# Performance work log

Hardware: AMD Instinct MI355X
Metric: run time of the kernel (lower is better)

Reference implementation:

```python
import jax, jax.numpy as jnp
import numpy as np

N, D, P = 131072, 128, 512
COMMIT_W = 0.1
ENT_LAMBDA = 200000.0


def setup_inputs() -> dict:
    key = jax.random.key(0)
    k1, k2 = jax.random.split(key)
    input_data = jax.random.normal(k1, (N, D), dtype=jnp.float32)
    # codebook init matches torch: uniform(-1/p, 1/p)
    codebook = jax.random.uniform(k2, (P, D), dtype=jnp.float32, minval=-1.0 / P, maxval=1.0 / P)
    return {"input_data": input_data, "codebook": codebook}


def _inv_cov(codebook):
    # full covariance of codebook rows (torch.no_grad -> stop_gradient)
    p, d = codebook.shape
    mu = codebook.mean(axis=0, keepdims=True)
    c = codebook - mu
    cov = (c.T @ c) / (p - 1) + 1e-3 * jnp.eye(d, dtype=codebook.dtype)
    return jax.lax.stop_gradient(jnp.linalg.inv(cov))


def reference(input_data, codebook):
    p, d = codebook.shape
    inv_cov = _inv_cov(codebook)

    # Mahalanobis distances via quadratic-form expansion (no [N,p,d] intermediate):
    xS = input_data @ inv_cov                      # [N, d]
    xq = jnp.sum(xS * input_data, axis=1)          # [N]
    cS = codebook @ inv_cov                        # [p, d]
    cq = jnp.sum(cS * codebook, axis=1)            # [p]
    distances = xq[:, None] - 2.0 * (xS @ codebook.T) + cq[None, :]  # [N, p]

    idx = jnp.argmin(distances, axis=1)            # [N]
    quantized = jnp.take(codebook, idx, axis=0)    # [N, d] (== one_hot @ codebook)

    def batch_mahal(x, y):
        diff = x - y
        return jnp.mean(jnp.sum((diff @ inv_cov) * diff, axis=1))

    codebook_loss = batch_mahal(jax.lax.stop_gradient(quantized), input_data)
    commitment_loss = COMMIT_W * batch_mahal(quantized, jax.lax.stop_gradient(input_data))

    # codebook usage entropy regularizer
    counts = jnp.zeros((p,), dtype=input_data.dtype).at[idx].add(1.0)
    probs = counts / (counts.sum() + 1e-8)
    entropy = -jnp.sum(probs * jnp.log(probs + 1e-8))
    codebook_loss = codebook_loss - ENT_LAMBDA * entropy

    # straight-through estimator
    quantized_st = input_data + jax.lax.stop_gradient(quantized - input_data)
    return quantized_st, commitment_loss, codebook_loss, idx
```

## Files before the change

kernel.cpp:

```cpp
#include <hip/hip_runtime.h>


typedef _Float16 half8 __attribute__((ext_vector_type(8)));
typedef float floatx4 __attribute__((ext_vector_type(4)));

#define NROWS 131072
#define DIM 128
#define NCODE 512
#define ND 16777216

#define WS_LH    0
#define WS_CH    32768
#define WS_W     163840
#define WS_SH    294912
#define WS_CQ    327680
#define WS_CNT   329728
#define WS_SUMS  346112

#define MFMA16(A, B, C) __builtin_amdgcn_mfma_f32_16x16x32_f16(A, B, C, 0, 0, 0)

__device__ __forceinline__ int moff(int row, int colh) {
  return row * 256 + ((((row & 7) << 4) ^ (colh * 2)));
}

__device__ __forceinline__ void stage4k(const char* src, char* ldsbase,
                                        int w, int lane) {
  __builtin_amdgcn_global_load_lds(
      (const __attribute__((address_space(1))) void*)(src + (w * 1024 + lane * 16)),
      (__attribute__((address_space(3))) void*)(ldsbase + w * 1024),
      16, 0, 0);
}

__global__ __launch_bounds__(256) void k_prep1(
    const float* __restrict__ cb, _Float16* __restrict__ Lh,
    unsigned* __restrict__ cnt, float* __restrict__ sums) {
  __shared__ float mu[128];
  __shared__ float red[256];
  __shared__ float colI[2][512];
  __shared__ float csh[2];

  const int t = threadIdx.x, b = blockIdx.x;
  const int j = t & 127, h = t >> 7;

  if (b < 8) {
    cnt[b * 512 + t] = 0u;
    cnt[b * 512 + 256 + t] = 0u;
  }
  if (b == 8) sums[t] = 0.f;

  float sm = 0.f, sf = 0.f;
  for (int p = 0; p < 256; ++p) {
    float v = cb[(h * 256 + p) * DIM + j];
    sm += v;
    sf += v * v;
  }
  red[t] = sm;
  for (int k = t; k < 1024; k += 256)
    colI[k >> 9][k & 511] = cb[(k & 511) * DIM + 2 * b + (k >> 9)];
  __syncthreads();
  if (t < 128) mu[t] = (red[t] + red[t + 128]) * (1.f / 512.f);
  __syncthreads();
  red[t] = sf - ((t < 128) ? 512.f * mu[t] * mu[t] : 0.f);
  __syncthreads();
  for (int k = 128; k > 0; k >>= 1) {
    if (t < k) red[t] += red[t + k];
    __syncthreads();
  }
  if (t == 0) {
    float tr = red[0] * (1.f / 511.f) + 0.128f;
    csh[0] = 128.f / tr;
    csh[1] = sqrtf(128.f / tr);
  }
  __syncthreads();
  const float c = csh[0], rc = csh[1];

  const int i = 2 * b + h;
  float g = 0.f;
  for (int q = 0; q < 512; ++q) g += colI[h][q] * cb[q * DIM + j];
  float lv = rc * (((i == j) ? (1.5f - 5e-4f * c) : 0.f) -
                   (c / 1022.f) * (g - 512.f * mu[i] * mu[j]));
  *(_Float16*)((char*)Lh + moff(i, j)) = (_Float16)lv;
}

__global__ __launch_bounds__(256) void k_prep2(
    const float* __restrict__ cb, const _Float16* __restrict__ Lh,
    _Float16* __restrict__ Ch, float* __restrict__ cqb) {
  __shared__ float cqpart[16][4];
  const int t = threadIdx.x;
  const int w = t >> 6, lane = t & 63, quad = lane >> 4, l16 = lane & 15;
  const int p0 = blockIdx.x * 16;

  half8 a[4];
#pragma unroll
  for (int ci = 0; ci < 4; ++ci) {
    const float4* v = (const float4*)(cb + (p0 + l16) * DIM + ci * 32 + quad * 8);
    float4 v0 = v[0], v1 = v[1];
    half8 hh;
    hh[0] = (_Float16)v0.x; hh[1] = (_Float16)v0.y;
    hh[2] = (_Float16)v0.z; hh[3] = (_Float16)v0.w;
    hh[4] = (_Float16)v1.x; hh[5] = (_Float16)v1.y;
    hh[6] = (_Float16)v1.z; hh[7] = (_Float16)v1.w;
    a[ci] = hh;
  }
  float sq[4] = {0.f, 0.f, 0.f, 0.f};
#pragma unroll
  for (int t2 = 0; t2 < 2; ++t2) {
    const int tile = w * 2 + t2;
    floatx4 s = {0.f, 0.f, 0.f, 0.f};
#pragma unroll
    for (int ci = 0; ci < 4; ++ci) {
      half8 bb = *(const half8*)((const char*)Lh +
                                 moff(tile * 16 + l16, ci * 32 + quad * 8));
      s = MFMA16(a[ci], bb, s);
    }
#pragma unroll
    for (int r = 0; r < 4; ++r) {
      *(_Float16*)((char*)Ch + moff(p0 + quad * 4 + r, tile * 16 + l16)) =
          (_Float16)s[r];
      sq[r] += s[r] * s[r];
    }
  }
#pragma unroll
  for (int r = 0; r < 4; ++r) {
    float v = sq[r];
    v += __shfl_xor(v, 1); v += __shfl_xor(v, 2);
    v += __shfl_xor(v, 4); v += __shfl_xor(v, 8);
    sq[r] = v;
  }
  if (l16 == 0)
#pragma unroll
    for (int r = 0; r < 4; ++r) cqpart[quad * 4 + r][w] = sq[r];
  __syncthreads();
  if (t < 16)
    cqb[p0 + t] = 1024.f - 0.5f * (cqpart[t][0] + cqpart[t][1] +
                                   cqpart[t][2] + cqpart[t][3]);
}

__global__ __launch_bounds__(256) void k_prep3(
    const _Float16* __restrict__ Lh, const _Float16* __restrict__ Ch,
    _Float16* __restrict__ W, _Float16* __restrict__ Sh) {
  const int t = threadIdx.x;
  const int w = t >> 6, lane = t & 63, quad = lane >> 4, l16 = lane & 15;
  const bool isW = blockIdx.x < 32;
  const int p0 = (isW ? blockIdx.x : (blockIdx.x - 32)) * 16;
  const char* Asrc = isW ? (const char*)Ch : (const char*)Lh;
  char* Dst = isW ? (char*)W : (char*)Sh;

  half8 a[4];
#pragma unroll
  for (int ci = 0; ci < 4; ++ci)
    a[ci] = *(const half8*)(Asrc + moff(p0 + l16, ci * 32 + quad * 8));
#pragma unroll
  for (int t2 = 0; t2 < 2; ++t2) {
    const int tile = w * 2 + t2;
    floatx4 s = {0.f, 0.f, 0.f, 0.f};
#pragma unroll
    for (int ci = 0; ci < 4; ++ci) {
      half8 bb = *(const half8*)((const char*)Lh +
                                 moff(tile * 16 + l16, ci * 32 + quad * 8));
      s = MFMA16(a[ci], bb, s);
    }
#pragma unroll
    for (int r = 0; r < 4; ++r)
      *(_Float16*)(Dst + moff(p0 + quad * 4 + r, tile * 16 + l16)) =
          (_Float16)s[r];
  }
}

__global__ __launch_bounds__(256, 3) void k_main(
    const float* __restrict__ X, const float* __restrict__ cb,
    const _Float16* __restrict__ Sh, const _Float16* __restrict__ W,
    const float* __restrict__ cqb, float* __restrict__ out,
    unsigned* __restrict__ cnt, float* __restrict__ sums) {
  __shared__ __align__(16) char Xs[32768];
  __shared__ __align__(16) char Bst[2][4096];

  const int tid = threadIdx.x;
  const int w = tid >> 6, lane = tid & 63;
  const int quad = lane >> 4, l16 = lane & 15;
  const int R0 = blockIdx.x * 128;
  const int rep = blockIdx.x & 7;
  const int r0 = w * 32;
  const int brot = (blockIdx.x >> 3) & 31;

  const char* ShB = (const char*)Sh;
  const char* WB = (const char*)W;

  {
    const float4* src = (const float4*)(X + (size_t)R0 * DIM);
#pragma unroll
    for (int it = 0; it < 8; ++it) {
      int g = it * 256 + tid;
      int row = g >> 4, c8 = g & 15;
      float4 v0 = src[g * 2];
      float4 v1 = src[g * 2 + 1];
      half8 hh;
      hh[0] = (_Float16)v0.x; hh[1] = (_Float16)v0.y;
      hh[2] = (_Float16)v0.z; hh[3] = (_Float16)v0.w;
      hh[4] = (_Float16)v1.x; hh[5] = (_Float16)v1.y;
      hh[6] = (_Float16)v1.z; hh[7] = (_Float16)v1.w;
      *(half8*)(Xs + moff(row, c8 * 8)) = hh;
    }
  }

  stage4k(ShB, Bst[0], w, lane);
  __syncthreads();

  half8 a0[4], a1[4];
#pragma unroll
  for (int ci = 0; ci < 4; ++ci) {
    a0[ci] = *(const half8*)(Xs + moff(r0 + l16, ci * 32 + quad * 8));
    a1[ci] = *(const half8*)(Xs + moff(r0 + 16 + l16, ci * 32 + quad * 8));
  }

  float y2 = 0.f;
  float m0[4] = {0.f, 0.f, 0.f, 0.f}, m1[4] = {0.f, 0.f, 0.f, 0.f};

  for (int v = 0; v < 40; ++v) {
    if (v < 39) {
      const char* nsrc = (v + 1 < 8)
                             ? (ShB + (size_t)(v + 1) * 4096)
                             : (WB + (size_t)((v + 1 - 8 + brot) & 31) * 4096);
      stage4k(nsrc, Bst[(v + 1) & 1], w, lane);
    }

    const char* lb = Bst[v & 1];
    half8 bb[4];
#pragma unroll
    for (int ci = 0; ci < 4; ++ci)
      bb[ci] = *(const half8*)(lb + moff(l16, ci * 32 + quad * 8));

    if (v < 8) {
      floatx4 s0a = {0.f, 0.f, 0.f, 0.f}, s0b = {0.f, 0.f, 0.f, 0.f};
      floatx4 s1a = {0.f, 0.f, 0.f, 0.f}, s1b = {0.f, 0.f, 0.f, 0.f};
      __builtin_amdgcn_s_setprio(1);
      s0a = MFMA16(a0[0], bb[0], s0a); s0b = MFMA16(a0[1], bb[1], s0b);
      s1a = MFMA16(a1[0], bb[0], s1a); s1b = MFMA16(a1[1], bb[1], s1b);
      s0a = MFMA16(a0[2], bb[2], s0a); s0b = MFMA16(a0[3], bb[3], s0b);
      s1a = MFMA16(a1[2], bb[2], s1a); s1b = MFMA16(a1[3], bb[3], s1b);
      __builtin_amdgcn_s_setprio(0);
      const int col = v * 16 + l16;
#pragma unroll
      for (int r = 0; r < 4; ++r) {
        float xv0 = (float)*(const _Float16*)(Xs + moff(r0 + quad * 4 + r, col));
        float xv1 = (float)*(const _Float16*)(Xs + moff(r0 + 16 + quad * 4 + r, col));
        y2 += (s0a[r] + s0b[r]) * xv0 + (s1a[r] + s1b[r]) * xv1;
      }
    } else {
      const int tt = (v - 8 + brot) & 31;
      const float iv = cqb[tt * 16 + l16];
      floatx4 s0a = {iv, iv, iv, iv}, s0b = {0.f, 0.f, 0.f, 0.f};
      floatx4 s1a = {iv, iv, iv, iv}, s1b = {0.f, 0.f, 0.f, 0.f};
      __builtin_amdgcn_s_setprio(1);
      s0a = MFMA16(a0[0], bb[0], s0a); s0b = MFMA16(a0[1], bb[1], s0b);
      s1a = MFMA16(a1[0], bb[0], s1a); s1b = MFMA16(a1[1], bb[1], s1b);
      s0a = MFMA16(a0[2], bb[2], s0a); s0b = MFMA16(a0[3], bb[3], s0b);
      s1a = MFMA16(a1[2], bb[2], s1a); s1b = MFMA16(a1[3], bb[3], s1b);
      __builtin_amdgcn_s_setprio(0);
      const unsigned tag = 511u - (unsigned)(tt * 16 + l16);
#pragma unroll
      for (int r = 0; r < 4; ++r) {
        float v0 = s0a[r] + s0b[r], v1 = s1a[r] + s1b[r];
        unsigned u0 = ((__float_as_uint(v0) + 0x100u) & 0xFFFFFE00u) | tag;
        unsigned u1 = ((__float_as_uint(v1) + 0x100u) & 0xFFFFFE00u) | tag;
        m0[r] = fmaxf(m0[r], __uint_as_float(u0));
        m1[r] = fmaxf(m1[r], __uint_as_float(u1));
      }
    }
    __syncthreads();
  }

#pragma unroll
  for (int r = 0; r < 4; ++r) {
#pragma unroll
    for (int msk = 1; msk < 16; msk <<= 1) {
      m0[r] = fmaxf(m0[r], __shfl_xor(m0[r], msk));
      m1[r] = fmaxf(m1[r], __shfl_xor(m1[r], msk));
    }
  }

  float contrib = y2;
  if (l16 == 0) {
#pragma unroll
    for (int r = 0; r < 4; ++r) {
      contrib -= 2.f * (__uint_as_float(__float_as_uint(m0[r]) & 0xFFFFFE00u) - 1024.f);
      contrib -= 2.f * (__uint_as_float(__float_as_uint(m1[r]) & 0xFFFFFE00u) - 1024.f);
    }
  }
#pragma unroll
  for (int msk = 1; msk < 64; msk <<= 1) contrib += __shfl_xor(contrib, msk);
  if (lane == 0) unsafeAtomicAdd(&sums[rep * 32], contrib);

  {
    const float4* cb4 = (const float4*)cb;
    float4* out4 = (float4*)out;
#pragma unroll
    for (int r = 0; r < 4; ++r) {
      const int j0 = 511 - (int)(__float_as_uint(m0[r]) & 511u);
      const int j1 = 511 - (int)(__float_as_uint(m1[r]) & 511u);
      const int row0 = R0 + r0 + quad * 4 + r, row1 = row0 + 16;
      out4[(size_t)row0 * 32 + l16 * 2]     = cb4[(size_t)j0 * 32 + l16 * 2];
      out4[(size_t)row0 * 32 + l16 * 2 + 1] = cb4[(size_t)j0 * 32 + l16 * 2 + 1];
      out4[(size_t)row1 * 32 + l16 * 2]     = cb4[(size_t)j1 * 32 + l16 * 2];
      out4[(size_t)row1 * 32 + l16 * 2 + 1] = cb4[(size_t)j1 * 32 + l16 * 2 + 1];
      if (l16 == 0) {
        out[ND + 2 + row0] = (float)j0;
        out[ND + 2 + row1] = (float)j1;
        atomicAdd(&cnt[rep * 512 + j0], 1u);
        atomicAdd(&cnt[rep * 512 + j1], 1u);
      }
    }
  }
}

__global__ void k_final(const unsigned* __restrict__ cnt,
                        const float* __restrict__ sums, float* __restrict__ out) {
  __shared__ double sd[256];
  int t = threadIdx.x;
  double e = 0.0;
  for (int c = t; c < NCODE; c += 256) {
    unsigned u = 0;
#pragma unroll
    for (int r = 0; r < 8; ++r) u += cnt[r * 512 + c];
    float p = (float)u * (1.0f / 131072.0f);
    e += (double)(p * logf(p + 1e-8f));
  }
  sd[t] = e;
  __syncthreads();
  for (int k = 128; k > 0; k >>= 1) {
    if (t < k) sd[t] += sd[t + k];
    __syncthreads();
  }
  if (t == 0) {
    double ent = -sd[0];
    float st = 0.f;
#pragma unroll
    for (int r = 0; r < 8; ++r) st += sums[r * 32];
    double M = (double)st / 131072.0;
    out[ND] = (float)(0.1 * M);
    out[ND + 1] = (float)(M - 200000.0 * ent);
  }
}

extern "C" void kernel_launch(void* const* d_in, const int* in_sizes, int n_in,
                              void* d_out, int out_size, void* d_ws, size_t ws_size,
                              hipStream_t stream) {
  const float* X = (const float*)d_in[0];
  const float* cb = (const float*)d_in[1];
  char* ws = (char*)d_ws;
  _Float16* Lh = (_Float16*)(ws + WS_LH);
  _Float16* Ch = (_Float16*)(ws + WS_CH);
  _Float16* W = (_Float16*)(ws + WS_W);
  _Float16* Sh = (_Float16*)(ws + WS_SH);
  float* cqb = (float*)(ws + WS_CQ);
  unsigned* cnt = (unsigned*)(ws + WS_CNT);
  float* sums = (float*)(ws + WS_SUMS);
  float* out = (float*)d_out;

  k_prep1<<<64, 256, 0, stream>>>(cb, Lh, cnt, sums);
  k_prep2<<<32, 256, 0, stream>>>(cb, Lh, Ch, cqb);
  k_prep3<<<40, 256, 0, stream>>>(Lh, Ch, W, Sh);
  k_main<<<1024, 256, 0, stream>>>(X, cb, Sh, W, cqb, out, cnt, sums);
  k_final<<<1, 256, 0, stream>>>(cnt, sums, out);
}
```

Measured before the change: 166.8 us.

## Stage full W codebook in LDS once per 1024-thread block and fuse prep kernels

The main kernel now uses 1024-thread blocks that load the whole 128 KB fp16 W matrix into LDS once, instead of double-buffering 4 KB tiles with a barrier every iteration. X rows go straight from global memory into registers, and the Sh quadratic term reads Sh and X directly from global memory. The second and third prep kernels are merged into one launch, which removes a launch and a dependency step. In exchange, 128 KB of LDS per block limits occupancy to one block per CU and gives 256 blocks in total. The merge also looks racy: W is computed from Ch in the same kernel that writes Ch, relying on the block's own rows, and it reads Lh rows that other blocks wrote in the previous kernel.

```diff
diff --git a/kernel.cpp b/kernel.cpp
--- a/kernel.cpp
+++ b/kernel.cpp
@@ -23,14 +23,6 @@
   return row * 256 + ((((row & 7) << 4) ^ (colh * 2)));
 }
 
-__device__ __forceinline__ void stage4k(const char* src, char* ldsbase,
-                                        int w, int lane) {
-  __builtin_amdgcn_global_load_lds(
-      (const __attribute__((address_space(1))) void*)(src + (w * 1024 + lane * 16)),
-      (__attribute__((address_space(3))) void*)(ldsbase + w * 1024),
-      16, 0, 0);
-}
-
 __global__ __launch_bounds__(256) void k_prep1(
     const float* __restrict__ cb, _Float16* __restrict__ Lh,
     unsigned* __restrict__ cnt, float* __restrict__ sums) {
@@ -82,12 +74,38 @@
   *(_Float16*)((char*)Lh + moff(i, j)) = (_Float16)lv;
 }
 
-__global__ __launch_bounds__(256) void k_prep2(
+__global__ __launch_bounds__(256) void k_prep23(
     const float* __restrict__ cb, const _Float16* __restrict__ Lh,
-    _Float16* __restrict__ Ch, float* __restrict__ cqb) {
+    _Float16* __restrict__ Ch, _Float16* __restrict__ W,
+    _Float16* __restrict__ Sh, float* __restrict__ cqb) {
   __shared__ float cqpart[16][4];
   const int t = threadIdx.x;
   const int w = t >> 6, lane = t & 63, quad = lane >> 4, l16 = lane & 15;
+
+  if (blockIdx.x >= 32) {
+    const int p0 = (blockIdx.x - 32) * 16;
+    half8 a[4];
+#pragma unroll
+    for (int ci = 0; ci < 4; ++ci)
+      a[ci] = *(const half8*)((const char*)Lh + moff(p0 + l16, ci * 32 + quad * 8));
+#pragma unroll
+    for (int t2 = 0; t2 < 2; ++t2) {
+      const int tile = w * 2 + t2;
+      floatx4 s = {0.f, 0.f, 0.f, 0.f};
+#pragma unroll
+      for (int ci = 0; ci < 4; ++ci) {
+        half8 bb = *(const half8*)((const char*)Lh +
+                                   moff(tile * 16 + l16, ci * 32 + quad * 8));
+        s = MFMA16(a[ci], bb, s);
+      }
+#pragma unroll
+      for (int r = 0; r < 4; ++r)
+        *(_Float16*)((char*)Sh + moff(p0 + quad * 4 + r, tile * 16 + l16)) =
+            (_Float16)s[r];
+    }
+    return;
+  }
+
   const int p0 = blockIdx.x * 16;
 
   half8 a[4];
@@ -134,22 +152,11 @@
   if (t < 16)
     cqb[p0 + t] = 1024.f - 0.5f * (cqpart[t][0] + cqpart[t][1] +
                                    cqpart[t][2] + cqpart[t][3]);
-}
-
-__global__ __launch_bounds__(256) void k_prep3(
-    const _Float16* __restrict__ Lh, const _Float16* __restrict__ Ch,
-    _Float16* __restrict__ W, _Float16* __restrict__ Sh) {
-  const int t = threadIdx.x;
-  const int w = t >> 6, lane = t & 63, quad = lane >> 4, l16 = lane & 15;
-  const bool isW = blockIdx.x < 32;
-  const int p0 = (isW ? blockIdx.x : (blockIdx.x - 32)) * 16;
-  const char* Asrc = isW ? (const char*)Ch : (const char*)Lh;
-  char* Dst = isW ? (char*)W : (char*)Sh;
-
-  half8 a[4];
+
+  half8 a2[4];
 #pragma unroll
   for (int ci = 0; ci < 4; ++ci)
-    a[ci] = *(const half8*)(Asrc + moff(p0 + l16, ci * 32 + quad * 8));
+    a2[ci] = *(const half8*)((const char*)Ch + moff(p0 + l16, ci * 32 + quad * 8));
 #pragma unroll
   for (int t2 = 0; t2 < 2; ++t2) {
     const int tile = w * 2 + t2;
@@ -158,116 +165,106 @@
     for (int ci = 0; ci < 4; ++ci) {
       half8 bb = *(const half8*)((const char*)Lh +
                                  moff(tile * 16 + l16, ci * 32 + quad * 8));
-      s = MFMA16(a[ci], bb, s);
+      s = MFMA16(a2[ci], bb, s);
     }
 #pragma unroll
     for (int r = 0; r < 4; ++r)
-      *(_Float16*)(Dst + moff(p0 + quad * 4 + r, tile * 16 + l16)) =
+      *(_Float16*)((char*)W + moff(p0 + quad * 4 + r, tile * 16 + l16)) =
           (_Float16)s[r];
   }
 }
 
-__global__ __launch_bounds__(256, 3) void k_main(
+__global__ __launch_bounds__(1024, 4) void k_main(
     const float* __restrict__ X, const float* __restrict__ cb,
     const _Float16* __restrict__ Sh, const _Float16* __restrict__ W,
     const float* __restrict__ cqb, float* __restrict__ out,
     unsigned* __restrict__ cnt, float* __restrict__ sums) {
-  __shared__ __align__(16) char Xs[32768];
-  __shared__ __align__(16) char Bst[2][4096];
+  __shared__ __align__(16) char Ws[131072];
 
   const int tid = threadIdx.x;
   const int w = tid >> 6, lane = tid & 63;
   const int quad = lane >> 4, l16 = lane & 15;
-  const int R0 = blockIdx.x * 128;
+  const int R0 = blockIdx.x * 512 + w * 32;
   const int rep = blockIdx.x & 7;
-  const int r0 = w * 32;
-  const int brot = (blockIdx.x >> 3) & 31;
-
+
+  half8 a0[4], a1[4];
+#pragma unroll
+  for (int ci = 0; ci < 4; ++ci) {
+    const float4* p0 = (const float4*)(X + (size_t)(R0 + l16) * DIM + ci * 32 + quad * 8);
+    float4 u0 = p0[0], u1 = p0[1];
+    half8 h;
+    h[0] = (_Float16)u0.x; h[1] = (_Float16)u0.y;
+    h[2] = (_Float16)u0.z; h[3] = (_Float16)u0.w;
+    h[4] = (_Float16)u1.x; h[5] = (_Float16)u1.y;
+    h[6] = (_Float16)u1.z; h[7] = (_Float16)u1.w;
+    a0[ci] = h;
+    const float4* p1 = (const float4*)(X + (size_t)(R0 + 16 + l16) * DIM + ci * 32 + quad * 8);
+    float4 w0 = p1[0], w1 = p1[1];
+    h[0] = (_Float16)w0.x; h[1] = (_Float16)w0.y;
+    h[2] = (_Float16)w0.z; h[3] = (_Float16)w0.w;
+    h[4] = (_Float16)w1.x; h[5] = (_Float16)w1.y;
+    h[6] = (_Float16)w1.z; h[7] = (_Float16)w1.w;
+    a1[ci] = h;
+  }
+
+  const char* WB = (const char*)W;
+#pragma unroll
+  for (int i = 0; i < 8; ++i)
+    __builtin_amdgcn_global_load_lds(
+        (const __attribute__((address_space(1))) void*)(WB + i * 16384 + w * 1024 + lane * 16),
+        (__attribute__((address_space(3))) void*)(Ws + i * 16384 + w * 1024),
+        16, 0, 0);
+
+  float y2 = 0.f;
   const char* ShB = (const char*)Sh;
-  const char* WB = (const char*)W;
-
-  {
-    const float4* src = (const float4*)(X + (size_t)R0 * DIM);
-#pragma unroll
-    for (int it = 0; it < 8; ++it) {
-      int g = it * 256 + tid;
-      int row = g >> 4, c8 = g & 15;
-      float4 v0 = src[g * 2];
-      float4 v1 = src[g * 2 + 1];
-      half8 hh;
-      hh[0] = (_Float16)v0.x; hh[1] = (_Float16)v0.y;
-      hh[2] = (_Float16)v0.z; hh[3] = (_Float16)v0.w;
-      hh[4] = (_Float16)v1.x; hh[5] = (_Float16)v1.y;
-      hh[6] = (_Float16)v1.z; hh[7] = (_Float16)v1.w;
-      *(half8*)(Xs + moff(row, c8 * 8)) = hh;
-    }
-  }
-
-  stage4k(ShB, Bst[0], w, lane);
-  __syncthreads();
-
-  half8 a0[4], a1[4];
-#pragma unroll
-  for (int ci = 0; ci < 4; ++ci) {
-    a0[ci] = *(const half8*)(Xs + moff(r0 + l16, ci * 32 + quad * 8));
-    a1[ci] = *(const half8*)(Xs + moff(r0 + 16 + l16, ci * 32 + quad * 8));
-  }
-
-  float y2 = 0.f;
+  for (int v = 0; v < 8; ++v) {
+    half8 bb[4];
+#pragma unroll
+    for (int ci = 0; ci < 4; ++ci)
+      bb[ci] = *(const half8*)(ShB + moff(v * 16 + l16, ci * 32 + quad * 8));
+    floatx4 s0a = {0.f, 0.f, 0.f, 0.f}, s0b = {0.f, 0.f, 0.f, 0.f};
+    floatx4 s1a = {0.f, 0.f, 0.f, 0.f}, s1b = {0.f, 0.f, 0.f, 0.f};
+    s0a = MFMA16(a0[0], bb[0], s0a); s0b = MFMA16(a0[1], bb[1], s0b);
+    s1a = MFMA16(a1[0], bb[0], s1a); s1b = MFMA16(a1[1], bb[1], s1b);
+    s0a = MFMA16(a0[2], bb[2], s0a); s0b = MFMA16(a0[3], bb[3], s0b);
+    s1a = MFMA16(a1[2], bb[2], s1a); s1b = MFMA16(a1[3], bb[3], s1b);
+    const int col = v * 16 + l16;
+#pragma unroll
+    for (int r = 0; r < 4; ++r) {
+      float xv0 = X[(size_t)(R0 + quad * 4 + r) * DIM + col];
+      float xv1 = X[(size_t)(R0 + 16 + quad * 4 + r) * DIM + col];
+      y2 += (s0a[r] + s0b[r]) * xv0 + (s1a[r] + s1b[r]) * xv1;
+    }
+  }
+
+  __syncthreads();
+
   float m0[4] = {0.f, 0.f, 0.f, 0.f}, m1[4] = {0.f, 0.f, 0.f, 0.f};
-
-  for (int v = 0; v < 40; ++v) {
-    if (v < 39) {
-      const char* nsrc = (v + 1 < 8)
-                             ? (ShB + (size_t)(v + 1) * 4096)
-                             : (WB + (size_t)((v + 1 - 8 + brot) & 31) * 4096);
-      stage4k(nsrc, Bst[(v + 1) & 1], w, lane);
-    }
-
-    const char* lb = Bst[v & 1];
+  float iv = cqb[l16];
+  for (int t = 0; t < 32; ++t) {
     half8 bb[4];
 #pragma unroll
     for (int ci = 0; ci < 4; ++ci)
-      bb[ci] = *(const half8*)(lb + moff(l16, ci * 32 + quad * 8));
-
-    if (v < 8) {
-      floatx4 s0a = {0.f, 0.f, 0.f, 0.f}, s0b = {0.f, 0.f, 0.f, 0.f};
-      floatx4 s1a = {0.f, 0.f, 0.f, 0.f}, s1b = {0.f, 0.f, 0.f, 0.f};
-      __builtin_amdgcn_s_setprio(1);
-      s0a = MFMA16(a0[0], bb[0], s0a); s0b = MFMA16(a0[1], bb[1], s0b);
-      s1a = MFMA16(a1[0], bb[0], s1a); s1b = MFMA16(a1[1], bb[1], s1b);
-      s0a = MFMA16(a0[2], bb[2], s0a); s0b = MFMA16(a0[3], bb[3], s0b);
-      s1a = MFMA16(a1[2], bb[2], s1a); s1b = MFMA16(a1[3], bb[3], s1b);
-      __builtin_amdgcn_s_setprio(0);
-      const int col = v * 16 + l16;
-#pragma unroll
-      for (int r = 0; r < 4; ++r) {
-        float xv0 = (float)*(const _Float16*)(Xs + moff(r0 + quad * 4 + r, col));
-        float xv1 = (float)*(const _Float16*)(Xs + moff(r0 + 16 + quad * 4 + r, col));
-        y2 += (s0a[r] + s0b[r]) * xv0 + (s1a[r] + s1b[r]) * xv1;
-      }
-    } else {
-      const int tt = (v - 8 + brot) & 31;
-      const float iv = cqb[tt * 16 + l16];
-      floatx4 s0a = {iv, iv, iv, iv}, s0b = {0.f, 0.f, 0.f, 0.f};
-      floatx4 s1a = {iv, iv, iv, iv}, s1b = {0.f, 0.f, 0.f, 0.f};
-      __builtin_amdgcn_s_setprio(1);
-      s0a = MFMA16(a0[0], bb[0], s0a); s0b = MFMA16(a0[1], bb[1], s0b);
-      s1a = MFMA16(a1[0], bb[0], s1a); s1b = MFMA16(a1[1], bb[1], s1b);
-      s0a = MFMA16(a0[2], bb[2], s0a); s0b = MFMA16(a0[3], bb[3], s0b);
-      s1a = MFMA16(a1[2], bb[2], s1a); s1b = MFMA16(a1[3], bb[3], s1b);
-      __builtin_amdgcn_s_setprio(0);
-      const unsigned tag = 511u - (unsigned)(tt * 16 + l16);
-#pragma unroll
-      for (int r = 0; r < 4; ++r) {
-        float v0 = s0a[r] + s0b[r], v1 = s1a[r] + s1b[r];
-        unsigned u0 = ((__float_as_uint(v0) + 0x100u) & 0xFFFFFE00u) | tag;
-        unsigned u1 = ((__float_as_uint(v1) + 0x100u) & 0xFFFFFE00u) | tag;
-        m0[r] = fmaxf(m0[r], __uint_as_float(u0));
-        m1[r] = fmaxf(m1[r], __uint_as_float(u1));
-      }
-    }
-    __syncthreads();
+      bb[ci] = *(const half8*)(Ws + moff(t * 16 + l16, ci * 32 + quad * 8));
+    float ivn = (t < 31) ? cqb[(t + 1) * 16 + l16] : 0.f;
+    floatx4 s0a = {iv, iv, iv, iv}, s0b = {0.f, 0.f, 0.f, 0.f};
+    floatx4 s1a = {iv, iv, iv, iv}, s1b = {0.f, 0.f, 0.f, 0.f};
+    __builtin_amdgcn_s_setprio(1);
+    s0a = MFMA16(a0[0], bb[0], s0a); s0b = MFMA16(a0[1], bb[1], s0b);
+    s1a = MFMA16(a1[0], bb[0], s1a); s1b = MFMA16(a1[1], bb[1], s1b);
+    s0a = MFMA16(a0[2], bb[2], s0a); s0b = MFMA16(a0[3], bb[3], s0b);
+    s1a = MFMA16(a1[2], bb[2], s1a); s1b = MFMA16(a1[3], bb[3], s1b);
+    __builtin_amdgcn_s_setprio(0);
+    const unsigned tag = 511u - (unsigned)(t * 16 + l16);
+#pragma unroll
+    for (int r = 0; r < 4; ++r) {
+      float v0 = s0a[r] + s0b[r], v1 = s1a[r] + s1b[r];
+      unsigned u0 = ((__float_as_uint(v0) + 0x100u) & 0xFFFFFE00u) | tag;
+      unsigned u1 = ((__float_as_uint(v1) + 0x100u) & 0xFFFFFE00u) | tag;
+      m0[r] = fmaxf(m0[r], __uint_as_float(u0));
+      m1[r] = fmaxf(m1[r], __uint_as_float(u1));
+    }
+    iv = ivn;
   }
 
 #pragma unroll
@@ -298,7 +295,7 @@
     for (int r = 0; r < 4; ++r) {
       const int j0 = 511 - (int)(__float_as_uint(m0[r]) & 511u);
       const int j1 = 511 - (int)(__float_as_uint(m1[r]) & 511u);
-      const int row0 = R0 + r0 + quad * 4 + r, row1 = row0 + 16;
+      const int row0 = R0 + quad * 4 + r, row1 = row0 + 16;
       out4[(size_t)row0 * 32 + l16 * 2]     = cb4[(size_t)j0 * 32 + l16 * 2];
       out4[(size_t)row0 * 32 + l16 * 2 + 1] = cb4[(size_t)j0 * 32 + l16 * 2 + 1];
       out4[(size_t)row1 * 32 + l16 * 2]     = cb4[(size_t)j1 * 32 + l16 * 2];
@@ -358,8 +355,7 @@
   float* out = (float*)d_out;
 
   k_prep1<<<64, 256, 0, stream>>>(cb, Lh, cnt, sums);
-  k_prep2<<<32, 256, 0, stream>>>(cb, Lh, Ch, cqb);
-  k_prep3<<<40, 256, 0, stream>>>(Lh, Ch, W, Sh);
-  k_main<<<1024, 256, 0, stream>>>(X, cb, Sh, W, cqb, out, cnt, sums);
+  k_prep23<<<40, 256, 0, stream>>>(cb, Lh, Ch, W, Sh, cqb);
+  k_main<<<256, 1024, 0, stream>>>(X, cb, Sh, W, cqb, out, cnt, sums);
   k_final<<<1, 256, 0, stream>>>(cnt, sums, out);
 }
```

Result: no change. 167.0 us (+0.1%).
